# Kernel tuning notes

Hardware: AMD Instinct MI355X
Metric: run time of the kernel (lower is better)

Reference implementation:

```python
import jax, jax.numpy as jnp
import numpy as np


def setup_inputs() -> dict:
    key = jax.random.key(0)
    ks = jax.random.split(key, 10)
    N, E = 50000, 1600000
    IN, H, OUT = 32, 64, 16
    x = jax.random.normal(ks[0], (N, IN), dtype=jnp.float32)
    edge_index = jax.random.randint(ks[1], (2, E), 0, N, dtype=jnp.int64)
    edge_attr = jax.random.normal(ks[2], (E, 3), dtype=jnp.float32)
    s1 = 1.0 / np.sqrt(2 * IN + 3)
    W1 = jax.random.uniform(ks[3], (2 * IN + 3, H), jnp.float32, -s1, s1)
    b1 = jax.random.uniform(ks[4], (H,), jnp.float32, -s1, s1)
    s2 = 1.0 / np.sqrt(H)
    W2 = jax.random.uniform(ks[5], (H, H), jnp.float32, -s2, s2)
    b2 = jax.random.uniform(ks[6], (H,), jnp.float32, -s2, s2)
    Wo = jax.random.uniform(ks[7], (H, OUT), jnp.float32, -s2, s2)
    bo = jax.random.uniform(ks[8], (OUT,), jnp.float32, -s2, s2)
    return {"x": x, "edge_index": edge_index, "edge_attr": edge_attr,
            "W1": W1, "b1": b1, "W2": W2, "b2": b2, "Wo": Wo, "bo": bo}


def reference(x, edge_index, edge_attr, W1, b1, W2, b2, Wo, bo):
    N = x.shape[0]
    src, dst = edge_index[0], edge_index[1]  # PyG: x_j = x[src], x_i = x[dst]
    x_i = x[dst]                      # [E, IN]
    x_j = x[src]                      # [E, IN]
    tmp = jnp.concatenate([x_i, x_j - x_i, edge_attr], axis=1)  # [E, 2*IN+3]
    h = jax.nn.relu(tmp @ W1 + b1)    # [E, H]
    msg = h @ W2 + b2                 # [E, H]
    # max-aggregate messages to destination nodes; empty segments -> 0 (PyG fill)
    agg = jax.ops.segment_max(msg, dst, num_segments=N)
    agg = jnp.where(jnp.isfinite(agg), agg, 0.0)
    out = jax.nn.sigmoid(agg @ Wo + bo)  # [N, OUT]
    return out
```

## Files before the change

kernel.cpp:

```cpp
#include <hip/hip_runtime.h>

#define IN_F 32
#define HID 64
#define OUTF 16
#define DPB 128
#define CAPB 5120
#define RSL 80
#define OVF_CAP 65536
#define ORD_NEG_INF 0x007FFFFFu

typedef _Float16 v8h __attribute__((ext_vector_type(8)));
typedef float v4f __attribute__((ext_vector_type(4)));

__device__ __forceinline__ unsigned ordenc(float v) {
  unsigned b = __float_as_uint(v);
  return (b & 0x80000000u) ? ~b : (b | 0x80000000u);
}
__device__ __forceinline__ float orddec(unsigned u) {
  unsigned b = (u & 0x80000000u) ? (u & 0x7FFFFFFFu) : ~u;
  return __uint_as_float(b);
}
__device__ __forceinline__ unsigned short f2h_bits(float f) {
  _Float16 h = (_Float16)f; unsigned short u; __builtin_memcpy(&u, &h, 2); return u;
}
__device__ __forceinline__ float h_bits2f(unsigned short u) {
  _Float16 h; __builtin_memcpy(&h, &u, 2); return (float)h;
}

__global__ __launch_bounds__(256) void p0_kernel(
    const int* __restrict__ ei,
    const float* __restrict__ x, const float* __restrict__ W1,
    const float* __restrict__ b1,
    float* __restrict__ P, _Float16* __restrict__ Q,
    unsigned* __restrict__ hist, int E, int N, int nSB, int NBKT)
{
  if (blockIdx.x < (unsigned)nSB) {
    __shared__ unsigned h[512];
    for (int i = threadIdx.x; i < NBKT; i += 256) h[i] = 0;
    __syncthreads();
    const int base = blockIdx.x * 1024;
    int d[4]; bool v[4];
#pragma unroll
    for (int i = 0; i < 4; ++i) {
      int e = base + i * 256 + threadIdx.x;
      v[i] = e < E;
      d[i] = ei[(size_t)E + (v[i] ? e : 0)];
    }
#pragma unroll
    for (int i = 0; i < 4; ++i)
      if (v[i]) atomicAdd(&h[d[i] >> 7], 1u);
    __syncthreads();
    for (int i = threadIdx.x; i < NBKT; i += 256)
      hist[(size_t)blockIdx.x * NBKT + i] = h[i];
    return;
  }
  const int lane = threadIdx.x & 63;
  float w1d[IN_F], w1b[IN_F];
#pragma unroll
  for (int c = 0; c < IN_F; ++c) {
    w1b[c] = W1[(IN_F + c) * HID + lane];
    w1d[c] = W1[c * HID + lane] - w1b[c];
  }
  const float b1v = b1[lane];
  int gw = __builtin_amdgcn_readfirstlane((((int)blockIdx.x - nSB) << 2) | (threadIdx.x >> 6));
  const int nwaves = 512 << 2;
  for (int n = gw; n < N; n += nwaves) {
    float p = b1v, q = 0.f;
#pragma unroll
    for (int c = 0; c < IN_F; ++c) {
      float xv = x[n * IN_F + c];
      p = fmaf(xv, w1d[c], p);
      q = fmaf(xv, w1b[c], q);
    }
    P[n * HID + lane] = p;
    Q[n * HID + lane] = (_Float16)q;
  }
}

__global__ __launch_bounds__(256) void scan_kernel(
    unsigned* __restrict__ hist, unsigned* __restrict__ totals,
    int nblk, int NBKT)
{
  __shared__ unsigned s[256];
  const int b = blockIdx.x;
  const int tid = threadIdx.x;
  unsigned running = 0;
  const int nch = (nblk + 255) >> 8;
  for (int c = 0; c < nch; ++c) {
    const int idx = c * 256 + tid;
    unsigned v = (idx < nblk) ? hist[(size_t)idx * NBKT + b] : 0u;
    s[tid] = v;
    __syncthreads();
#pragma unroll
    for (int off = 1; off < 256; off <<= 1) {
      unsigned t = (tid >= off) ? s[tid - off] : 0u;
      __syncthreads();
      s[tid] += t;
      __syncthreads();
    }
    const unsigned incl = s[tid];
    const unsigned tot = s[255];
    if (idx < nblk) hist[(size_t)idx * NBKT + b] = running + (incl - v);
    running += tot;
    __syncthreads();
  }
  if (tid == 0) totals[b] = running;
}

__global__ __launch_bounds__(256) void p1_kernel(
    const int* __restrict__ ei, const float* __restrict__ ea,
    const unsigned* __restrict__ hist,
    uint2* __restrict__ cu, unsigned char* __restrict__ cdlo,
    uint4* __restrict__ ovf, int* __restrict__ ovf_cnt,
    int E, int NBKT)
{
  __shared__ unsigned h2[512];
  for (int i = threadIdx.x; i < NBKT; i += 256) h2[i] = 0;
  __syncthreads();
  const int base = blockIdx.x * 1024;
  int s[4], d[4]; bool v[4];
#pragma unroll
  for (int i = 0; i < 4; ++i) {
    int e = base + i * 256 + threadIdx.x;
    v[i] = e < E;
    int ec = v[i] ? e : 0;
    s[i] = ei[ec];
    d[i] = ei[(size_t)E + ec];
  }
  float a0[4], a1[4], a2[4];
#pragma unroll
  for (int i = 0; i < 4; ++i) {
    int ec = v[i] ? (base + i * 256 + threadIdx.x) : 0;
    a0[i] = ea[ec * 3 + 0]; a1[i] = ea[ec * 3 + 1]; a2[i] = ea[ec * 3 + 2];
  }
#pragma unroll
  for (int i = 0; i < 4; ++i) {
    if (!v[i]) continue;
    const int b = d[i] >> 7;
    const unsigned r = atomicAdd(&h2[b], 1u);
    const unsigned pos = hist[(size_t)blockIdx.x * NBKT + b] + r;
    uint2 pay;
    pay.x = (unsigned)s[i] | ((unsigned)f2h_bits(a0[i]) << 16);
    pay.y = (unsigned)f2h_bits(a1[i]) | ((unsigned)f2h_bits(a2[i]) << 16);
    if (pos < CAPB) {
      cu[(size_t)b * CAPB + pos] = pay;
      cdlo[(size_t)b * CAPB + pos] = (unsigned char)(d[i] & (DPB - 1));
    } else {
      int oi = atomicAdd(ovf_cnt, 1);
      if (oi < OVF_CAP) ovf[oi] = make_uint4(pay.x, pay.y, (unsigned)d[i], 0u);
    }
  }
}

__global__ __launch_bounds__(512) void p2_kernel(
    const uint2* __restrict__ cu, const unsigned char* __restrict__ cdlo,
    const unsigned* __restrict__ totals,
    uint2* __restrict__ rec, int* __restrict__ cnt,
    uint4* __restrict__ ovf, int* __restrict__ ovf_cnt, int N)
{
  __shared__ int c[DPB];
  const int b = blockIdx.x;
  const int tid = threadIdx.x;
  if (tid < DPB) c[tid] = 0;
  __syncthreads();
  const int nE = (int)min(totals[b], (unsigned)CAPB);
  for (int i = tid; i < nE; i += 512) {
    const uint2 pay = cu[(size_t)b * CAPB + i];
    const int dlo = cdlo[(size_t)b * CAPB + i];
    const int r = atomicAdd(&c[dlo], 1);
    const int d = b * DPB + dlo;
    if (r < RSL) rec[(size_t)d * RSL + r] = pay;
    else {
      int oi = atomicAdd(ovf_cnt, 1);
      if (oi < OVF_CAP) ovf[oi] = make_uint4(pay.x, pay.y, (unsigned)d, 0u);
    }
  }
  __syncthreads();
  if (tid < DPB) {
    const int d = b * DPB + tid;
    if (d < N) cnt[d] = c[tid];
  }
}

__global__ __launch_bounds__(256) void bucket_kernel(
    const uint2* __restrict__ rec, const int* __restrict__ cnt,
    const float* __restrict__ W1, const float* __restrict__ W2,
    const float* __restrict__ P, const _Float16* __restrict__ Q,
    unsigned* __restrict__ agg, int N)
{
  __shared__ __align__(16) _Float16 hB[4][16][72];

  const int wave = threadIdx.x >> 6;
  const int lane = threadIdx.x & 63;
  const int quad = lane >> 4;
  const int eidx = lane & 15;
  const int mych = ((eidx >> 2) << 4) + (quad << 2) + (eidx & 3);

  v8h a_frag[4][2];
#pragma unroll
  for (int t = 0; t < 4; ++t)
#pragma unroll
    for (int ks = 0; ks < 2; ++ks)
#pragma unroll
      for (int j = 0; j < 8; ++j)
        a_frag[t][ks][j] = (_Float16)W2[(ks * 32 + quad * 8 + j) * HID + t * 16 + eidx];

  const float w1c0 = W1[(2 * IN_F + 0) * HID + lane];
  const float w1c1 = W1[(2 * IN_F + 1) * HID + lane];
  const float w1c2 = W1[(2 * IN_F + 2) * HID + lane];

  const int gwave = __builtin_amdgcn_readfirstlane((blockIdx.x << 2) | wave);
  const int nw = gridDim.x << 2;

  int d = gwave;
  if (d >= N) return;

  int m; uint2 r0, r1; float pP;
  auto prefetch = [&](int dd) {
    m = min(cnt[dd], RSL);
    if (lane < m) r0 = rec[(size_t)dd * RSL + lane];
    if (m > 64) {
      if (64 + lane < m) r1 = rec[(size_t)dd * RSL + 64 + lane];
    }
    pP = P[(size_t)dd * HID + lane];
  };

  prefetch(d);

  while (d < N) {
    const int dn = d + nw;
    const int m_cur = m;
    const float pvl = pP;
    uint2 ra = r0, rb = r1;

    if (m_cur > 0) {
      {
        const int lm = m_cur - 1;
        unsigned rlx, rly;
        if (lm < 64) {
          rlx = (unsigned)__builtin_amdgcn_readlane((int)ra.x, lm);
          rly = (unsigned)__builtin_amdgcn_readlane((int)ra.y, lm);
        } else {
          rlx = (unsigned)__builtin_amdgcn_readlane((int)rb.x, lm & 63);
          rly = (unsigned)__builtin_amdgcn_readlane((int)rb.y, lm & 63);
        }
        if (lane >= m_cur)      { ra.x = rlx; ra.y = rly; }
        if (lane + 64 >= m_cur) { rb.x = rlx; rb.y = rly; }
      }

      float qvA[8], qvB[8];
#pragma unroll
      for (int i = 0; i < 8; ++i) {
        unsigned sx = (unsigned)__builtin_amdgcn_readlane((int)ra.x, i) & 0xFFFFu;
        qvA[i] = (float)Q[(size_t)sx * HID + lane];
      }
#pragma unroll
      for (int i = 0; i < 8; ++i) {
        unsigned sx = (unsigned)__builtin_amdgcn_readlane((int)ra.x, 8 + i) & 0xFFFFu;
        qvB[i] = (float)Q[(size_t)sx * HID + lane];
      }

      if (dn < N) prefetch(dn);

      float maxv[4][4];
#pragma unroll
      for (int t = 0; t < 4; ++t)
#pragma unroll
        for (int r = 0; r < 4; ++r) maxv[t][r] = -INFINITY;

      const int ntile = (m_cur + 15) >> 4;
      const int noct = ntile << 1;
      for (int tb = 0; tb < ntile; ++tb) {
        const unsigned rsx = (tb < 4) ? ra.x : rb.x;
        const unsigned rsy = (tb < 4) ? ra.y : rb.y;
        const int b16 = (tb & 3) << 4;

#pragma unroll
        for (int i = 0; i < 8; ++i) {
          const unsigned rx = (unsigned)__builtin_amdgcn_readlane((int)rsx, b16 + i);
          const unsigned ry = (unsigned)__builtin_amdgcn_readlane((int)rsy, b16 + i);
          float pre = pvl + qvA[i];
          pre = fmaf(h_bits2f((unsigned short)(rx >> 16)), w1c0, pre);
          pre = fmaf(h_bits2f((unsigned short)(ry & 0xFFFFu)), w1c1, pre);
          pre = fmaf(h_bits2f((unsigned short)(ry >> 16)), w1c2, pre);
          hB[wave][i][lane] = (_Float16)fmaxf(pre, 0.f);
        }
        {
          const int o = 2 * tb + 2;
          if (o < noct) {
            const unsigned rox = (o < 8) ? ra.x : rb.x;
            const int bo = (o & 7) << 3;
#pragma unroll
            for (int i = 0; i < 8; ++i) {
              unsigned sx = (unsigned)__builtin_amdgcn_readlane((int)rox, bo + i) & 0xFFFFu;
              qvA[i] = (float)Q[(size_t)sx * HID + lane];
            }
          }
        }
#pragma unroll
        for (int i = 0; i < 8; ++i) {
          const unsigned rx = (unsigned)__builtin_amdgcn_readlane((int)rsx, b16 + 8 + i);
          const unsigned ry = (unsigned)__builtin_amdgcn_readlane((int)rsy, b16 + 8 + i);
          float pre = pvl + qvB[i];
          pre = fmaf(h_bits2f((unsigned short)(rx >> 16)), w1c0, pre);
          pre = fmaf(h_bits2f((unsigned short)(ry & 0xFFFFu)), w1c1, pre);
          pre = fmaf(h_bits2f((unsigned short)(ry >> 16)), w1c2, pre);
          hB[wave][8 + i][lane] = (_Float16)fmaxf(pre, 0.f);
        }
        {
          const int o = 2 * tb + 3;
          if (o < noct) {
            const unsigned rox = (o < 8) ? ra.x : rb.x;
            const int bo = (o & 7) << 3;
#pragma unroll
            for (int i = 0; i < 8; ++i) {
              unsigned sx = (unsigned)__builtin_amdgcn_readlane((int)rox, bo + i) & 0xFFFFu;
              qvB[i] = (float)Q[(size_t)sx * HID + lane];
            }
          }
        }
        __builtin_amdgcn_wave_barrier();

        const v8h bf0 = *(const v8h*)&hB[wave][eidx][quad * 8];
        const v8h bf1 = *(const v8h*)&hB[wave][eidx][32 + quad * 8];
#pragma unroll
        for (int t = 0; t < 4; ++t) {
          v4f acc = (v4f){0.f, 0.f, 0.f, 0.f};
          acc = __builtin_amdgcn_mfma_f32_16x16x32_f16(a_frag[t][0], bf0, acc, 0, 0, 0);
          acc = __builtin_amdgcn_mfma_f32_16x16x32_f16(a_frag[t][1], bf1, acc, 0, 0, 0);
#pragma unroll
          for (int r = 0; r < 4; ++r) maxv[t][r] = fmaxf(maxv[t][r], acc[r]);
        }
        __builtin_amdgcn_wave_barrier();
      }

#pragma unroll
      for (int t = 0; t < 4; ++t)
#pragma unroll
        for (int r = 0; r < 4; ++r) {
          float v = maxv[t][r];
          v = fmaxf(v, __shfl_xor(v, 1, 64));
          v = fmaxf(v, __shfl_xor(v, 2, 64));
          v = fmaxf(v, __shfl_xor(v, 4, 64));
          v = fmaxf(v, __shfl_xor(v, 8, 64));
          maxv[t][r] = v;
        }
      float val = maxv[0][0];
#pragma unroll
      for (int t = 0; t < 4; ++t)
#pragma unroll
        for (int r = 0; r < 4; ++r)
          val = (eidx == t * 4 + r) ? maxv[t][r] : val;
      agg[(size_t)d * HID + mych] = ordenc(val);
    } else {
      if (dn < N) prefetch(dn);
      agg[(size_t)d * HID + lane] = ORD_NEG_INF;
    }
    d = dn;
  }
}

__global__ __launch_bounds__(256) void overflow_kernel(
    const uint4* __restrict__ ovf, const int* __restrict__ ovf_cnt,
    const float* __restrict__ W1, const float* __restrict__ W2,
    const float* __restrict__ P, const _Float16* __restrict__ Q,
    unsigned* __restrict__ agg)
{
  __shared__ float hsh[4][HID];
  const int wave = threadIdx.x >> 6;
  const int lane = threadIdx.x & 63;

  int M = *ovf_cnt;
  if (M > OVF_CAP) M = OVF_CAP;
  if (M == 0) return;

  float w2r[HID];
#pragma unroll
  for (int j = 0; j < HID; ++j) w2r[j] = W2[j * HID + lane];
  const float w1c0 = W1[(2 * IN_F + 0) * HID + lane];
  const float w1c1 = W1[(2 * IN_F + 1) * HID + lane];
  const float w1c2 = W1[(2 * IN_F + 2) * HID + lane];

  const int gwave = __builtin_amdgcn_readfirstlane((blockIdx.x << 2) | wave);
  const int nw = gridDim.x << 2;
  for (int k = gwave; k < M; k += nw) {
    const uint4 o = ovf[k];
    const int s = (int)(o.x & 0xFFFFu);
    const int d = (int)o.z;
    float pre = P[(size_t)d * HID + lane] + (float)Q[(size_t)s * HID + lane];
    pre = fmaf(h_bits2f((unsigned short)(o.x >> 16)), w1c0, pre);
    pre = fmaf(h_bits2f((unsigned short)(o.y & 0xFFFFu)), w1c1, pre);
    pre = fmaf(h_bits2f((unsigned short)(o.y >> 16)), w1c2, pre);
    hsh[wave][lane] = fmaxf(pre, 0.f);
    __builtin_amdgcn_wave_barrier();
    float mv = 0.f;
#pragma unroll
    for (int j = 0; j < HID; ++j) mv = fmaf(hsh[wave][j], w2r[j], mv);
    atomicMax(&agg[(size_t)d * HID + lane], ordenc(mv));
    __builtin_amdgcn_wave_barrier();
  }
}

__global__ __launch_bounds__(256) void out_kernel(
    const unsigned* __restrict__ agg,
    const float* __restrict__ b2,
    const float* __restrict__ Wo, const float* __restrict__ bo,
    float* __restrict__ out, int N)
{
  __shared__ float Wos[HID * OUTF];
  __shared__ float bos[OUTF];
  __shared__ float b2s[HID];
  __shared__ float aggs[16][HID + 1];

  for (int i = threadIdx.x; i < HID * OUTF; i += 256) Wos[i] = Wo[i];
  if (threadIdx.x < OUTF) bos[threadIdx.x] = bo[threadIdx.x];
  if (threadIdx.x < HID) b2s[threadIdx.x] = b2[threadIdx.x];
  __syncthreads();

  const int nodeBase = blockIdx.x * 16;
  {
    int ln = threadIdx.x >> 4;
    int k0 = (threadIdx.x & 15) * 4;
    int n = nodeBase + ln;
    if (n < N) {
      const uint4 u = *(const uint4*)&agg[(size_t)n * HID + k0];
      aggs[ln][k0 + 0] = (u.x == ORD_NEG_INF) ? 0.f : orddec(u.x) + b2s[k0 + 0];
      aggs[ln][k0 + 1] = (u.y == ORD_NEG_INF) ? 0.f : orddec(u.y) + b2s[k0 + 1];
      aggs[ln][k0 + 2] = (u.z == ORD_NEG_INF) ? 0.f : orddec(u.z) + b2s[k0 + 2];
      aggs[ln][k0 + 3] = (u.w == ORD_NEG_INF) ? 0.f : orddec(u.w) + b2s[k0 + 3];
    }
  }
  __syncthreads();
  {
    int ln = threadIdx.x >> 4;
    int o = threadIdx.x & 15;
    int n = nodeBase + ln;
    if (n < N) {
      float acc = bos[o];
#pragma unroll
      for (int k = 0; k < HID; ++k) acc = fmaf(aggs[ln][k], Wos[k * OUTF + o], acc);
      out[n * OUTF + o] = 1.f / (1.f + __expf(-acc));
    }
  }
}

extern "C" void kernel_launch(void* const* d_in, const int* in_sizes, int n_in,
                              void* d_out, int out_size, void* d_ws, size_t ws_size,
                              hipStream_t stream) {
  const float* x  = (const float*)d_in[0];
  const int*   ei = (const int*)d_in[1];
  const float* ea = (const float*)d_in[2];
  const float* W1 = (const float*)d_in[3];
  const float* b1 = (const float*)d_in[4];
  const float* W2 = (const float*)d_in[5];
  const float* b2 = (const float*)d_in[6];
  const float* Wo = (const float*)d_in[7];
  const float* bo = (const float*)d_in[8];
  float* out = (float*)d_out;

  const int N = in_sizes[0] / IN_F;
  const int E = in_sizes[1] / 2;
  const int NBKT = (N + DPB - 1) / DPB;
  const int nSB  = (E + 1023) / 1024;

  char* w = (char*)d_ws;
  auto align16 = [](size_t v) { return (v + 15) & ~(size_t)15; };
  float*     Pp   = (float*)w;       w += align16((size_t)N * HID * 4);
  _Float16*  Qp   = (_Float16*)w;    w += align16((size_t)N * HID * 2);
  unsigned*  agg  = (unsigned*)w;    w += align16((size_t)N * HID * 4);
  uint2*     rec  = (uint2*)w;       w += align16((size_t)N * RSL * 8);
  uint2*     cu   = (uint2*)w;       w += align16((size_t)NBKT * CAPB * 8);
  unsigned*  hist = (unsigned*)w;    w += align16((size_t)nSB * NBKT * 4);
  unsigned*  tot  = (unsigned*)w;    w += align16((size_t)NBKT * 4);
  int*       cnt  = (int*)w;         w += align16((size_t)N * 4);
  unsigned char* cdlo = (unsigned char*)w; w += align16((size_t)NBKT * CAPB);
  int*   ovf_cnt  = (int*)w;         w += 16;
  uint4*     ovf  = (uint4*)w;

  hipMemsetAsync(ovf_cnt, 0, 16, stream);

  p0_kernel<<<nSB + 512, 256, 0, stream>>>(ei, x, W1, b1, Pp, Qp, hist, E, N, nSB, NBKT);
  scan_kernel<<<NBKT, 256, 0, stream>>>(hist, tot, nSB, NBKT);
  p1_kernel<<<nSB, 256, 0, stream>>>(ei, ea, hist, cu, cdlo, ovf, ovf_cnt, E, NBKT);
  p2_kernel<<<NBKT, 512, 0, stream>>>(cu, cdlo, tot, rec, cnt, ovf, ovf_cnt, N);
  bucket_kernel<<<4096, 256, 0, stream>>>(rec, cnt, W1, W2, Pp, Qp, agg, N);
  overflow_kernel<<<256, 256, 0, stream>>>(ovf, ovf_cnt, W1, W2, Pp, Qp, agg);
  out_kernel<<<(N + 15) / 16, 256, 0, stream>>>(agg, b2, Wo, bo, out, N);
}
```

Baseline: 264.9 us.

## Enlarge histogram/scatter blocks, assign contiguous node groups per wave, skip padded edges

The histogram and scatter kernels now handle 4096 edges per block instead of 1024. This cuts the number of blocks and shrinks the per-block histogram matrix that the scan kernel walks. The bucket kernel gives each wave four consecutive destination nodes with a matching grid size, replacing the grid-stride loop. It also skips Q gathers and layer-1 math for padding lanes beyond the edge count, filling padded rows with the last valid h value. The trade-offs are less parallelism in p0 and p1, extra predication, and a longer serial loop per block in those phases.

```diff
diff --git a/kernel.cpp b/kernel.cpp
--- a/kernel.cpp
+++ b/kernel.cpp
@@ -6,6 +6,7 @@
 #define DPB 128
 #define CAPB 5120
 #define RSL 80
+#define EPB 4096
 #define OVF_CAP 65536
 #define ORD_NEG_INF 0x007FFFFFu
 
@@ -38,17 +39,21 @@
     __shared__ unsigned h[512];
     for (int i = threadIdx.x; i < NBKT; i += 256) h[i] = 0;
     __syncthreads();
-    const int base = blockIdx.x * 1024;
-    int d[4]; bool v[4];
-#pragma unroll
-    for (int i = 0; i < 4; ++i) {
-      int e = base + i * 256 + threadIdx.x;
-      v[i] = e < E;
-      d[i] = ei[(size_t)E + (v[i] ? e : 0)];
-    }
-#pragma unroll
-    for (int i = 0; i < 4; ++i)
-      if (v[i]) atomicAdd(&h[d[i] >> 7], 1u);
+    const int base = blockIdx.x * EPB;
+#pragma unroll 1
+    for (int r = 0; r < 4; ++r) {
+      const int b2 = base + r * 1024;
+      int dd[4]; bool vv[4];
+#pragma unroll
+      for (int i = 0; i < 4; ++i) {
+        int e = b2 + i * 256 + threadIdx.x;
+        vv[i] = e < E;
+        dd[i] = ei[(size_t)E + (vv[i] ? e : 0)];
+      }
+#pragma unroll
+      for (int i = 0; i < 4; ++i)
+        if (vv[i]) atomicAdd(&h[dd[i] >> 7], 1u);
+    }
     __syncthreads();
     for (int i = threadIdx.x; i < NBKT; i += 256)
       hist[(size_t)blockIdx.x * NBKT + i] = h[i];
@@ -117,37 +122,41 @@
   __shared__ unsigned h2[512];
   for (int i = threadIdx.x; i < NBKT; i += 256) h2[i] = 0;
   __syncthreads();
-  const int base = blockIdx.x * 1024;
-  int s[4], d[4]; bool v[4];
-#pragma unroll
-  for (int i = 0; i < 4; ++i) {
-    int e = base + i * 256 + threadIdx.x;
-    v[i] = e < E;
-    int ec = v[i] ? e : 0;
-    s[i] = ei[ec];
-    d[i] = ei[(size_t)E + ec];
-  }
-  float a0[4], a1[4], a2[4];
-#pragma unroll
-  for (int i = 0; i < 4; ++i) {
-    int ec = v[i] ? (base + i * 256 + threadIdx.x) : 0;
-    a0[i] = ea[ec * 3 + 0]; a1[i] = ea[ec * 3 + 1]; a2[i] = ea[ec * 3 + 2];
-  }
-#pragma unroll
-  for (int i = 0; i < 4; ++i) {
-    if (!v[i]) continue;
-    const int b = d[i] >> 7;
-    const unsigned r = atomicAdd(&h2[b], 1u);
-    const unsigned pos = hist[(size_t)blockIdx.x * NBKT + b] + r;
-    uint2 pay;
-    pay.x = (unsigned)s[i] | ((unsigned)f2h_bits(a0[i]) << 16);
-    pay.y = (unsigned)f2h_bits(a1[i]) | ((unsigned)f2h_bits(a2[i]) << 16);
-    if (pos < CAPB) {
-      cu[(size_t)b * CAPB + pos] = pay;
-      cdlo[(size_t)b * CAPB + pos] = (unsigned char)(d[i] & (DPB - 1));
-    } else {
-      int oi = atomicAdd(ovf_cnt, 1);
-      if (oi < OVF_CAP) ovf[oi] = make_uint4(pay.x, pay.y, (unsigned)d[i], 0u);
+  const int base = blockIdx.x * EPB;
+#pragma unroll 1
+  for (int r = 0; r < 4; ++r) {
+    const int b2 = base + r * 1024;
+    int s[4], d[4]; bool v[4];
+#pragma unroll
+    for (int i = 0; i < 4; ++i) {
+      int e = b2 + i * 256 + threadIdx.x;
+      v[i] = e < E;
+      int ec = v[i] ? e : 0;
+      s[i] = ei[ec];
+      d[i] = ei[(size_t)E + ec];
+    }
+    float a0[4], a1[4], a2[4];
+#pragma unroll
+    for (int i = 0; i < 4; ++i) {
+      int ec = v[i] ? (b2 + i * 256 + threadIdx.x) : 0;
+      a0[i] = ea[ec * 3 + 0]; a1[i] = ea[ec * 3 + 1]; a2[i] = ea[ec * 3 + 2];
+    }
+#pragma unroll
+    for (int i = 0; i < 4; ++i) {
+      if (!v[i]) continue;
+      const int b = d[i] >> 7;
+      const unsigned rr = atomicAdd(&h2[b], 1u);
+      const unsigned pos = hist[(size_t)blockIdx.x * NBKT + b] + rr;
+      uint2 pay;
+      pay.x = (unsigned)s[i] | ((unsigned)f2h_bits(a0[i]) << 16);
+      pay.y = (unsigned)f2h_bits(a1[i]) | ((unsigned)f2h_bits(a2[i]) << 16);
+      if (pos < CAPB) {
+        cu[(size_t)b * CAPB + pos] = pay;
+        cdlo[(size_t)b * CAPB + pos] = (unsigned char)(d[i] & (DPB - 1));
+      } else {
+        int oi = atomicAdd(ovf_cnt, 1);
+        if (oi < OVF_CAP) ovf[oi] = make_uint4(pay.x, pay.y, (unsigned)d[i], 0u);
+      }
     }
   }
 }
@@ -210,10 +219,10 @@
   const float w1c2 = W1[(2 * IN_F + 2) * HID + lane];
 
   const int gwave = __builtin_amdgcn_readfirstlane((blockIdx.x << 2) | wave);
-  const int nw = gridDim.x << 2;
-
-  int d = gwave;
+
+  int d = gwave * 4;
   if (d >= N) return;
+  const int dend = min(d + 4, N);
 
   int m; uint2 r0, r1; float pP;
   auto prefetch = [&](int dd) {
@@ -227,40 +236,32 @@
 
   prefetch(d);
 
-  while (d < N) {
-    const int dn = d + nw;
+  while (d < dend) {
+    const int dn = d + 1;
     const int m_cur = m;
     const float pvl = pP;
-    uint2 ra = r0, rb = r1;
+    const uint2 ra = r0, rb = r1;
 
     if (m_cur > 0) {
+      float qvA[8], qvB[8];
       {
-        const int lm = m_cur - 1;
-        unsigned rlx, rly;
-        if (lm < 64) {
-          rlx = (unsigned)__builtin_amdgcn_readlane((int)ra.x, lm);
-          rly = (unsigned)__builtin_amdgcn_readlane((int)ra.y, lm);
-        } else {
-          rlx = (unsigned)__builtin_amdgcn_readlane((int)rb.x, lm & 63);
-          rly = (unsigned)__builtin_amdgcn_readlane((int)rb.y, lm & 63);
-        }
-        if (lane >= m_cur)      { ra.x = rlx; ra.y = rly; }
-        if (lane + 64 >= m_cur) { rb.x = rlx; rb.y = rly; }
+        const int c0 = m_cur < 8 ? m_cur : 8;
+        const int c1 = m_cur < 8 ? 0 : (m_cur < 16 ? m_cur - 8 : 8);
+#pragma unroll
+        for (int i = 0; i < 8; ++i)
+          if (i < c0) {
+            unsigned sx = (unsigned)__builtin_amdgcn_readlane((int)ra.x, i) & 0xFFFFu;
+            qvA[i] = (float)Q[(size_t)sx * HID + lane];
+          }
+#pragma unroll
+        for (int i = 0; i < 8; ++i)
+          if (i < c1) {
+            unsigned sx = (unsigned)__builtin_amdgcn_readlane((int)ra.x, 8 + i) & 0xFFFFu;
+            qvB[i] = (float)Q[(size_t)sx * HID + lane];
+          }
       }
 
-      float qvA[8], qvB[8];
-#pragma unroll
-      for (int i = 0; i < 8; ++i) {
-        unsigned sx = (unsigned)__builtin_amdgcn_readlane((int)ra.x, i) & 0xFFFFu;
-        qvA[i] = (float)Q[(size_t)sx * HID + lane];
-      }
-#pragma unroll
-      for (int i = 0; i < 8; ++i) {
-        unsigned sx = (unsigned)__builtin_amdgcn_readlane((int)ra.x, 8 + i) & 0xFFFFu;
-        qvB[i] = (float)Q[(size_t)sx * HID + lane];
-      }
-
-      if (dn < N) prefetch(dn);
+      if (dn < dend) prefetch(dn);
 
       float maxv[4][4];
 #pragma unroll
@@ -269,55 +270,77 @@
         for (int r = 0; r < 4; ++r) maxv[t][r] = -INFINITY;
 
       const int ntile = (m_cur + 15) >> 4;
-      const int noct = ntile << 1;
       for (int tb = 0; tb < ntile; ++tb) {
         const unsigned rsx = (tb < 4) ? ra.x : rb.x;
         const unsigned rsy = (tb < 4) ? ra.y : rb.y;
         const int b16 = (tb & 3) << 4;
+        const int rem = m_cur - (tb << 4);
+        const int n0 = rem < 8 ? rem : 8;
+        const int n1 = rem < 8 ? 0 : (rem < 16 ? rem - 8 : 8);
+        _Float16 hlast = (_Float16)0.f;
 
 #pragma unroll
         for (int i = 0; i < 8; ++i) {
-          const unsigned rx = (unsigned)__builtin_amdgcn_readlane((int)rsx, b16 + i);
-          const unsigned ry = (unsigned)__builtin_amdgcn_readlane((int)rsy, b16 + i);
-          float pre = pvl + qvA[i];
-          pre = fmaf(h_bits2f((unsigned short)(rx >> 16)), w1c0, pre);
-          pre = fmaf(h_bits2f((unsigned short)(ry & 0xFFFFu)), w1c1, pre);
-          pre = fmaf(h_bits2f((unsigned short)(ry >> 16)), w1c2, pre);
-          hB[wave][i][lane] = (_Float16)fmaxf(pre, 0.f);
+          if (i < n0) {
+            const unsigned rx = (unsigned)__builtin_amdgcn_readlane((int)rsx, b16 + i);
+            const unsigned ry = (unsigned)__builtin_amdgcn_readlane((int)rsy, b16 + i);
+            float pre = pvl + qvA[i];
+            pre = fmaf(h_bits2f((unsigned short)(rx >> 16)), w1c0, pre);
+            pre = fmaf(h_bits2f((unsigned short)(ry & 0xFFFFu)), w1c1, pre);
+            pre = fmaf(h_bits2f((unsigned short)(ry >> 16)), w1c2, pre);
+            _Float16 hv = (_Float16)fmaxf(pre, 0.f);
+            hB[wave][i][lane] = hv;
+            hlast = hv;
+          }
         }
         {
           const int o = 2 * tb + 2;
-          if (o < noct) {
+          const int co = m_cur - (o << 3);
+          if (co > 0) {
+            const int cc = co < 8 ? co : 8;
             const unsigned rox = (o < 8) ? ra.x : rb.x;
             const int bo = (o & 7) << 3;
 #pragma unroll
-            for (int i = 0; i < 8; ++i) {
-              unsigned sx = (unsigned)__builtin_amdgcn_readlane((int)rox, bo + i) & 0xFFFFu;
-              qvA[i] = (float)Q[(size_t)sx * HID + lane];
-            }
+            for (int i = 0; i < 8; ++i)
+              if (i < cc) {
+                unsigned sx = (unsigned)__builtin_amdgcn_readlane((int)rox, bo + i) & 0xFFFFu;
+                qvA[i] = (float)Q[(size_t)sx * HID + lane];
+              }
           }
         }
 #pragma unroll
         for (int i = 0; i < 8; ++i) {
-          const unsigned rx = (unsigned)__builtin_amdgcn_readlane((int)rsx, b16 + 8 + i);
-          const unsigned ry = (unsigned)__builtin_amdgcn_readlane((int)rsy, b16 + 8 + i);
-          float pre = pvl + qvB[i];
-          pre = fmaf(h_bits2f((unsigned short)(rx >> 16)), w1c0, pre);
-          pre = fmaf(h_bits2f((unsigned short)(ry & 0xFFFFu)), w1c1, pre);
-          pre = fmaf(h_bits2f((unsigned short)(ry >> 16)), w1c2, pre);
-          hB[wave][8 + i][lane] = (_Float16)fmaxf(pre, 0.f);
+          if (i < n1) {
+            const unsigned rx = (unsigned)__builtin_amdgcn_readlane((int)rsx, b16 + 8 + i);
+            const unsigned ry = (unsigned)__builtin_amdgcn_readlane((int)rsy, b16 + 8 + i);
+            float pre = pvl + qvB[i];
+            pre = fmaf(h_bits2f((unsigned short)(rx >> 16)), w1c0, pre);
+            pre = fmaf(h_bits2f((unsigned short)(ry & 0xFFFFu)), w1c1, pre);
+            pre = fmaf(h_bits2f((unsigned short)(ry >> 16)), w1c2, pre);
+            _Float16 hv = (_Float16)fmaxf(pre, 0.f);
+            hB[wave][8 + i][lane] = hv;
+            hlast = hv;
+          }
         }
         {
           const int o = 2 * tb + 3;
-          if (o < noct) {
+          const int co = m_cur - (o << 3);
+          if (co > 0) {
+            const int cc = co < 8 ? co : 8;
             const unsigned rox = (o < 8) ? ra.x : rb.x;
             const int bo = (o & 7) << 3;
 #pragma unroll
-            for (int i = 0; i < 8; ++i) {
-              unsigned sx = (unsigned)__builtin_amdgcn_readlane((int)rox, bo + i) & 0xFFFFu;
-              qvB[i] = (float)Q[(size_t)sx * HID + lane];
-            }
+            for (int i = 0; i < 8; ++i)
+              if (i < cc) {
+                unsigned sx = (unsigned)__builtin_amdgcn_readlane((int)rox, bo + i) & 0xFFFFu;
+                qvB[i] = (float)Q[(size_t)sx * HID + lane];
+              }
           }
+        }
+        if (rem < 16) {
+#pragma unroll
+          for (int i = 0; i < 16; ++i)
+            if (i >= rem) hB[wave][i][lane] = hlast;
         }
         __builtin_amdgcn_wave_barrier();
 
@@ -353,7 +376,7 @@
           val = (eidx == t * 4 + r) ? maxv[t][r] : val;
       agg[(size_t)d * HID + mych] = ordenc(val);
     } else {
-      if (dn < N) prefetch(dn);
+      if (dn < dend) prefetch(dn);
       agg[(size_t)d * HID + lane] = ORD_NEG_INF;
     }
     d = dn;
@@ -461,7 +484,7 @@
   const int N = in_sizes[0] / IN_F;
   const int E = in_sizes[1] / 2;
   const int NBKT = (N + DPB - 1) / DPB;
-  const int nSB  = (E + 1023) / 1024;
+  const int nSB  = (E + EPB - 1) / EPB;
 
   char* w = (char*)d_ws;
   auto align16 = [](size_t v) { return (v + 15) & ~(size_t)15; };
@@ -483,7 +506,7 @@
   scan_kernel<<<NBKT, 256, 0, stream>>>(hist, tot, nSB, NBKT);
   p1_kernel<<<nSB, 256, 0, stream>>>(ei, ea, hist, cu, cdlo, ovf, ovf_cnt, E, NBKT);
   p2_kernel<<<NBKT, 512, 0, stream>>>(cu, cdlo, tot, rec, cnt, ovf, ovf_cnt, N);
-  bucket_kernel<<<4096, 256, 0, stream>>>(rec, cnt, W1, W2, Pp, Qp, agg, N);
+  bucket_kernel<<<(N + 15) / 16, 256, 0, stream>>>(rec, cnt, W1, W2, Pp, Qp, agg, N);
   overflow_kernel<<<256, 256, 0, stream>>>(ovf, ovf_cnt, W1, W2, Pp, Qp, agg);
   out_kernel<<<(N + 15) / 16, 256, 0, stream>>>(agg, b2, Wo, bo, out, N);
 }
```

New measurement: 364.4 us. +37.6%, slower.
